# Performance work log

Hardware: AMD Instinct MI355X
Metric: run time of the kernel (lower is better)

Reference implementation:

```python
import jax, jax.numpy as jnp
import numpy as np

M_MODES = 12
N_PHOTONS = 6  # input_state = [1]*6 + [0]*6


def _glynn_signs(n):
    # All delta in {+1,-1}^n with delta_0 = +1 : 2^(n-1) sign vectors.
    k = np.arange(2 ** (n - 1))
    bits = (k[:, None] >> np.arange(n - 1)[None, :]) & 1  # [S, n-1]
    signs = np.concatenate([np.ones((k.size, 1)), 1.0 - 2.0 * bits], axis=1)
    parity = np.prod(signs, axis=1)  # [S]
    return jnp.asarray(signs, jnp.float32), jnp.asarray(parity, jnp.float32)


def _batched_permanent(Msub):
    # Glynn formula: perm(M) = 2^(1-n) * sum_delta prod(delta) * prod_j sum_i delta_i M_ij
    n = Msub.shape[-1]
    signs, parity = _glynn_signs(n)
    signs = signs.astype(Msub.dtype)
    # [..., S, n] row-sums under each sign vector
    rowsums = jnp.einsum('sn,...nj->...sj', signs, Msub)
    prods = jnp.prod(rowsums, axis=-1)  # [..., S]
    perm = jnp.einsum('s,...s->...', parity.astype(Msub.dtype), prods)
    return perm / (2.0 ** (n - 1))


def _feature_unitaries(x, A, B):
    # U(x) = A @ diag(exp(i x)) @ B  (phase-shifter layer between fixed interferometers)
    ph = jnp.exp(1j * x.astype(jnp.complex64))  # [N, m]
    return jnp.einsum('ab,nb,bc->nac', A, ph, B)  # [N, m, m]


def setup_inputs() -> dict:
    key = jax.random.key(0)
    k1, k2, k3, k4 = jax.random.split(key, 4)
    x1 = jax.random.normal(k1, (384, M_MODES), jnp.float32)
    x2 = jax.random.normal(k2, (384, M_MODES), jnp.float32)
    # Fixed Haar-random unitaries for the interferometer meshes
    rng = np.random.default_rng(0)
    A = np.linalg.qr(rng.normal(size=(M_MODES, M_MODES)) + 1j * rng.normal(size=(M_MODES, M_MODES)))[0]
    B = np.linalg.qr(rng.normal(size=(M_MODES, M_MODES)) + 1j * rng.normal(size=(M_MODES, M_MODES)))[0]
    return {
        'x1': x1, 'x2': x2,
        'A_re': jnp.asarray(A.real, jnp.float32), 'A_im': jnp.asarray(A.imag, jnp.float32),
        'B_re': jnp.asarray(B.real, jnp.float32), 'B_im': jnp.asarray(B.imag, jnp.float32),
    }


def reference(x1, x2, A_re, A_im, B_re, B_im):
    A = (A_re + 1j * A_im).astype(jnp.complex64)
    B = (B_re + 1j * B_im).astype(jnp.complex64)
    U1 = _feature_unitaries(x1, A, B)  # [N1, m, m]
    U2 = _feature_unitaries(x2, A, B)  # [N2, m, m]
    n = N_PHOTONS
    # W = U(x2)^dag U(x1); amplitude = perm(W[s_idx, s_idx]) with s_idx = first n modes
    # (input_state = [1]*n + [0]*(m-n), all factorials = 1)
    Wsub = jnp.einsum('jka,ikb->ijab', jnp.conj(U2[:, :, :n]), U1[:, :, :n])  # [N1,N2,n,n]
    amp = _batched_permanent(Wsub)  # [N1, N2] complex
    K = jnp.abs(amp) ** 2
    return K.astype(jnp.float32)
```

## Files before the change

### kernel.cpp

```cpp
#include <hip/hip_runtime.h>


#define NS 384
#define MM 12
#define NP 6
#define TS 16
#define SV_STRIDE 148

struct c32 { float x, y; };

__device__ __forceinline__ c32 cmul(c32 a, c32 b) {
    c32 r;
    r.x = fmaf(a.x, b.x, -a.y * b.y);
    r.y = fmaf(a.x, b.y,  a.y * b.x);
    return r;
}

__global__ void build_V_kernel(const float* __restrict__ x1,
                               const float* __restrict__ x2,
                               const float* __restrict__ Ar, const float* __restrict__ Ai,
                               const float* __restrict__ Br, const float* __restrict__ Bi,
                               float* __restrict__ V1, float* __restrict__ V2c) {
    int idx = blockIdx.x * blockDim.x + threadIdx.x;
    if (idx >= 2 * NS * NP * 2) return;
    int ah = idx & 1;
    int rest = idx >> 1;
    int c = rest % NP; rest /= NP;
    int s = rest % NS;
    int half = rest / NS;
    const float* x = half ? x2 : x1;

    float tr[MM], ti[MM];
#pragma unroll
    for (int b = 0; b < MM; ++b) {
        float sv, cv;
        __sincosf(x[s * MM + b], &sv, &cv);
        float br = Br[b * MM + c], bi = Bi[b * MM + c];
        tr[b] = fmaf(cv, br, -sv * bi);
        ti[b] = fmaf(cv, bi,  sv * br);
    }

    float* V = half ? V2c : V1;
    float sgn = half ? -1.f : 1.f;
#pragma unroll
    for (int a0 = 0; a0 < NP; ++a0) {
        int a = ah * NP + a0;
        float ure = 0.f, uim = 0.f;
#pragma unroll
        for (int b = 0; b < MM; ++b) {
            float ar = Ar[a * MM + b], ai = Ai[a * MM + b];
            ure = fmaf(ar, tr[b], fmaf(-ai, ti[b], ure));
            uim = fmaf(ar, ti[b], fmaf( ai, tr[b], uim));
        }
        int off = ((s * MM + a) * NP + c) * 2;
        V[off]     = ure;
        V[off + 1] = sgn * uim;
    }
}

__device__ __forceinline__ c32 tree_prod(const c32 rs[NP]) {
    c32 p01 = cmul(rs[0], rs[1]);
    c32 p23 = cmul(rs[2], rs[3]);
    c32 p45 = cmul(rs[4], rs[5]);
    return cmul(cmul(p01, p23), p45);
}

__global__ __launch_bounds__(256) void perm_kernel(const float* __restrict__ V1g,
                                                   const float* __restrict__ V2g,
                                                   float* __restrict__ out) {
    __shared__ __align__(16) float sV1[TS * SV_STRIDE];
    __shared__ __align__(16) float sV2[TS * SV_STRIDE];
    const int i0 = blockIdx.y * TS;
    const int j0 = blockIdx.x * TS;
    const int tid = threadIdx.x;

    for (int idx = tid; idx < 2 * TS * 36; idx += 256) {
        int which = idx >= TS * 36;
        int rem = which ? idx - TS * 36 : idx;
        int s = rem / 36, q = rem - s * 36;
        const float* src = which ? (V2g + (j0 + s) * 144) : (V1g + (i0 + s) * 144);
        float4 v = *(const float4*)(src + q * 4);
        float* dst = (which ? sV2 : sV1) + s * SV_STRIDE + q * 4;
        *(float4*)dst = v;
    }
    __syncthreads();

    const int tx = tid & 15, ty = tid >> 4;
    const float* v1 = sV1 + ty * SV_STRIDE;
    const float* v2 = sV2 + tx * SV_STRIDE;

    c32 W[NP][NP];
#pragma unroll
    for (int a = 0; a < NP; ++a)
#pragma unroll
        for (int b = 0; b < NP; ++b) { W[a][b].x = 0.f; W[a][b].y = 0.f; }

#pragma unroll
    for (int k = 0; k < MM; ++k) {
        float4 p1[3], p2[3];
#pragma unroll
        for (int q = 0; q < 3; ++q) {
            p1[q] = *(const float4*)(v1 + k * 12 + q * 4);
            p2[q] = *(const float4*)(v2 + k * 12 + q * 4);
        }
        const float* f1 = (const float*)p1;
        const float* f2 = (const float*)p2;
#pragma unroll
        for (int a = 0; a < NP; ++a) {
            float a2x = f2[2 * a], a2y = f2[2 * a + 1];
#pragma unroll
            for (int b = 0; b < NP; ++b) {
                float a1x = f1[2 * b], a1y = f1[2 * b + 1];
                W[a][b].x = fmaf(a2x, a1x, fmaf(-a2y, a1y, W[a][b].x));
                W[a][b].y = fmaf(a2x, a1y, fmaf( a2y, a1x, W[a][b].y));
            }
        }
    }

    c32 base[NP];
#pragma unroll
    for (int b = 0; b < NP; ++b) {
        base[b] = W[0][b];
#pragma unroll
        for (int a = 1; a < NP; ++a) { base[b].x += W[a][b].x; base[b].y += W[a][b].y; }
    }

    c32 rs[4][NP];
#pragma unroll
    for (int b = 0; b < NP; ++b) {
        rs[0][b] = base[b];
        rs[1][b].x = fmaf(-2.f, W[4][b].x, base[b].x);
        rs[1][b].y = fmaf(-2.f, W[4][b].y, base[b].y);
        rs[2][b].x = fmaf(-2.f, W[5][b].x, base[b].x);
        rs[2][b].y = fmaf(-2.f, W[5][b].y, base[b].y);
        rs[3][b].x = fmaf(-2.f, W[5][b].x, rs[1][b].x);
        rs[3][b].y = fmaf(-2.f, W[5][b].y, rs[1][b].y);
    }
    float accx[4], accy[4];
#pragma unroll
    for (int ch = 0; ch < 4; ++ch) {
        c32 p = tree_prod(rs[ch]);
        accx[ch] = p.x; accy[ch] = p.y;
    }

    unsigned st = 0;
#pragma unroll
    for (int u = 1; u < 8; ++u) {
        const int bitpos = __builtin_ctz(u);
        const int r = bitpos + 1;
        float cf = ((st >> bitpos) & 1) ? 2.f : -2.f;
        st ^= (1u << bitpos);
        float sgn_u = (u & 1) ? -1.f : 1.f;
#pragma unroll
        for (int ch = 0; ch < 4; ++ch) {
#pragma unroll
            for (int b = 0; b < NP; ++b) {
                rs[ch][b].x = fmaf(cf, W[r][b].x, rs[ch][b].x);
                rs[ch][b].y = fmaf(cf, W[r][b].y, rs[ch][b].y);
            }
            c32 p = tree_prod(rs[ch]);
            accx[ch] = fmaf(sgn_u, p.x, accx[ch]);
            accy[ch] = fmaf(sgn_u, p.y, accy[ch]);
        }
    }

    float ax = accx[0] - accx[1] - accx[2] + accx[3];
    float ay = accy[0] - accy[1] - accy[2] + accy[3];
    float K = fmaf(ax, ax, ay * ay) * (1.f / 1024.f);
    out[(i0 + ty) * NS + (j0 + tx)] = K;
}

extern "C" void kernel_launch(void* const* d_in, const int* in_sizes, int n_in,
                              void* d_out, int out_size, void* d_ws, size_t ws_size,
                              hipStream_t stream) {
    const float* x1 = (const float*)d_in[0];
    const float* x2 = (const float*)d_in[1];
    const float* Ar = (const float*)d_in[2];
    const float* Ai = (const float*)d_in[3];
    const float* Br = (const float*)d_in[4];
    const float* Bi = (const float*)d_in[5];
    float* out = (float*)d_out;

    float* V1  = (float*)d_ws;
    float* V2c = V1 + NS * MM * NP * 2;

    int total = 2 * NS * NP * 2;
    build_V_kernel<<<(total + 255) / 256, 256, 0, stream>>>(x1, x2, Ar, Ai, Br, Bi, V1, V2c);

    dim3 grid(NS / TS, NS / TS);
    perm_kernel<<<grid, 256, 0, stream>>>(V1, V2c, out);
}
```

Baseline: 80.73 us.

## Use packed float2 FMA vectors and widen build_V parallelism to one thread per element

Rewrites the complex arithmetic in both kernels with 2-wide float vector types and elementwise FMA, so the compiler can emit packed FP32 instructions (v_pk_fma_f32 on CDNA). This is meant to roughly halve the VALU instruction count in the permanent and Gram accumulation loops. The build_V kernel now uses one thread per output element instead of one per half-row, giving more parallelism at the cost of recomputing sincos and the B product per thread. The packed operations may need extra register moves for the swizzled operands, which could eat into the saving.

```diff
diff --git a/kernel.cpp b/kernel.cpp
--- a/kernel.cpp
+++ b/kernel.cpp
@@ -1,5 +1,7 @@
 #include <hip/hip_runtime.h>
 
+
+typedef float v2f __attribute__((ext_vector_type(2)));
 
 #define NS 384
 #define MM 12
@@ -7,13 +9,13 @@
 #define TS 16
 #define SV_STRIDE 148
 
-struct c32 { float x, y; };
-
-__device__ __forceinline__ c32 cmul(c32 a, c32 b) {
-    c32 r;
-    r.x = fmaf(a.x, b.x, -a.y * b.y);
-    r.y = fmaf(a.x, b.y,  a.y * b.x);
-    return r;
+__device__ __forceinline__ v2f cmul(v2f a, v2f b) {
+    v2f r = (v2f){a.x, a.x} * b;
+    return __builtin_elementwise_fma((v2f){a.y, a.y}, (v2f){-b.y, b.x}, r);
+}
+__device__ __forceinline__ v2f cmac(v2f acc, v2f a, v2f b) {
+    acc = __builtin_elementwise_fma((v2f){a.x, a.x}, b, acc);
+    return __builtin_elementwise_fma((v2f){a.y, a.y}, (v2f){-b.y, b.x}, acc);
 }
 
 __global__ void build_V_kernel(const float* __restrict__ x1,
@@ -22,46 +24,33 @@
                                const float* __restrict__ Br, const float* __restrict__ Bi,
                                float* __restrict__ V1, float* __restrict__ V2c) {
     int idx = blockIdx.x * blockDim.x + threadIdx.x;
-    if (idx >= 2 * NS * NP * 2) return;
-    int ah = idx & 1;
-    int rest = idx >> 1;
-    int c = rest % NP; rest /= NP;
-    int s = rest % NS;
-    int half = rest / NS;
+    if (idx >= 2 * NS * MM * NP) return;
+    int c = idx % NP;  int rest = idx / NP;
+    int a = rest % MM; rest /= MM;
+    int s = rest % NS; int half = rest / NS;
     const float* x = half ? x2 : x1;
 
-    float tr[MM], ti[MM];
+    v2f u = {0.f, 0.f};
 #pragma unroll
     for (int b = 0; b < MM; ++b) {
         float sv, cv;
         __sincosf(x[s * MM + b], &sv, &cv);
-        float br = Br[b * MM + c], bi = Bi[b * MM + c];
-        tr[b] = fmaf(cv, br, -sv * bi);
-        ti[b] = fmaf(cv, bi,  sv * br);
+        v2f ph = {cv, sv};
+        v2f Bv = {Br[b * MM + c], Bi[b * MM + c]};
+        v2f t  = cmul(ph, Bv);
+        v2f Av = {Ar[a * MM + b], Ai[a * MM + b]};
+        u = cmac(u, Av, t);
     }
-
     float* V = half ? V2c : V1;
-    float sgn = half ? -1.f : 1.f;
-#pragma unroll
-    for (int a0 = 0; a0 < NP; ++a0) {
-        int a = ah * NP + a0;
-        float ure = 0.f, uim = 0.f;
-#pragma unroll
-        for (int b = 0; b < MM; ++b) {
-            float ar = Ar[a * MM + b], ai = Ai[a * MM + b];
-            ure = fmaf(ar, tr[b], fmaf(-ai, ti[b], ure));
-            uim = fmaf(ar, ti[b], fmaf( ai, tr[b], uim));
-        }
-        int off = ((s * MM + a) * NP + c) * 2;
-        V[off]     = ure;
-        V[off + 1] = sgn * uim;
-    }
+    int off = ((s * MM + a) * NP + c) * 2;
+    V[off]     = u.x;
+    V[off + 1] = half ? -u.y : u.y;
 }
 
-__device__ __forceinline__ c32 tree_prod(const c32 rs[NP]) {
-    c32 p01 = cmul(rs[0], rs[1]);
-    c32 p23 = cmul(rs[2], rs[3]);
-    c32 p45 = cmul(rs[4], rs[5]);
+__device__ __forceinline__ v2f tree_prod(const v2f rs[NP]) {
+    v2f p01 = cmul(rs[0], rs[1]);
+    v2f p23 = cmul(rs[2], rs[3]);
+    v2f p45 = cmul(rs[4], rs[5]);
     return cmul(cmul(p01, p23), p45);
 }
 
@@ -89,59 +78,46 @@
     const float* v1 = sV1 + ty * SV_STRIDE;
     const float* v2 = sV2 + tx * SV_STRIDE;
 
-    c32 W[NP][NP];
+    v2f W[NP][NP];
 #pragma unroll
     for (int a = 0; a < NP; ++a)
 #pragma unroll
-        for (int b = 0; b < NP; ++b) { W[a][b].x = 0.f; W[a][b].y = 0.f; }
+        for (int b = 0; b < NP; ++b) W[a][b] = (v2f){0.f, 0.f};
 
 #pragma unroll
     for (int k = 0; k < MM; ++k) {
-        float4 p1[3], p2[3];
+        const v2f* c1 = (const v2f*)(v1 + k * 12);
+        const v2f* c2 = (const v2f*)(v2 + k * 12);
+        v2f a1[NP], a2[NP];
 #pragma unroll
-        for (int q = 0; q < 3; ++q) {
-            p1[q] = *(const float4*)(v1 + k * 12 + q * 4);
-            p2[q] = *(const float4*)(v2 + k * 12 + q * 4);
-        }
-        const float* f1 = (const float*)p1;
-        const float* f2 = (const float*)p2;
+        for (int b = 0; b < NP; ++b) { a1[b] = c1[b]; a2[b] = c2[b]; }
 #pragma unroll
-        for (int a = 0; a < NP; ++a) {
-            float a2x = f2[2 * a], a2y = f2[2 * a + 1];
+        for (int a = 0; a < NP; ++a)
 #pragma unroll
-            for (int b = 0; b < NP; ++b) {
-                float a1x = f1[2 * b], a1y = f1[2 * b + 1];
-                W[a][b].x = fmaf(a2x, a1x, fmaf(-a2y, a1y, W[a][b].x));
-                W[a][b].y = fmaf(a2x, a1y, fmaf( a2y, a1x, W[a][b].y));
-            }
-        }
+            for (int b = 0; b < NP; ++b)
+                W[a][b] = cmac(W[a][b], a2[a], a1[b]);
     }
 
-    c32 base[NP];
+    v2f base[NP];
 #pragma unroll
     for (int b = 0; b < NP; ++b) {
         base[b] = W[0][b];
 #pragma unroll
-        for (int a = 1; a < NP; ++a) { base[b].x += W[a][b].x; base[b].y += W[a][b].y; }
+        for (int a = 1; a < NP; ++a) base[b] += W[a][b];
     }
 
-    c32 rs[4][NP];
+    v2f rs[4][NP];
 #pragma unroll
     for (int b = 0; b < NP; ++b) {
+        v2f m2 = {-2.f, -2.f};
         rs[0][b] = base[b];
-        rs[1][b].x = fmaf(-2.f, W[4][b].x, base[b].x);
-        rs[1][b].y = fmaf(-2.f, W[4][b].y, base[b].y);
-        rs[2][b].x = fmaf(-2.f, W[5][b].x, base[b].x);
-        rs[2][b].y = fmaf(-2.f, W[5][b].y, base[b].y);
-        rs[3][b].x = fmaf(-2.f, W[5][b].x, rs[1][b].x);
-        rs[3][b].y = fmaf(-2.f, W[5][b].y, rs[1][b].y);
+        rs[1][b] = __builtin_elementwise_fma(m2, W[4][b], base[b]);
+        rs[2][b] = __builtin_elementwise_fma(m2, W[5][b], base[b]);
+        rs[3][b] = __builtin_elementwise_fma(m2, W[5][b], rs[1][b]);
     }
-    float accx[4], accy[4];
+    v2f acc[4];
 #pragma unroll
-    for (int ch = 0; ch < 4; ++ch) {
-        c32 p = tree_prod(rs[ch]);
-        accx[ch] = p.x; accy[ch] = p.y;
-    }
+    for (int ch = 0; ch < 4; ++ch) acc[ch] = tree_prod(rs[ch]);
 
     unsigned st = 0;
 #pragma unroll
@@ -151,22 +127,20 @@
         float cf = ((st >> bitpos) & 1) ? 2.f : -2.f;
         st ^= (1u << bitpos);
         float sgn_u = (u & 1) ? -1.f : 1.f;
+        v2f cfv = {cf, cf};
+        v2f sgv = {sgn_u, sgn_u};
 #pragma unroll
         for (int ch = 0; ch < 4; ++ch) {
 #pragma unroll
-            for (int b = 0; b < NP; ++b) {
-                rs[ch][b].x = fmaf(cf, W[r][b].x, rs[ch][b].x);
-                rs[ch][b].y = fmaf(cf, W[r][b].y, rs[ch][b].y);
-            }
-            c32 p = tree_prod(rs[ch]);
-            accx[ch] = fmaf(sgn_u, p.x, accx[ch]);
-            accy[ch] = fmaf(sgn_u, p.y, accy[ch]);
+            for (int b = 0; b < NP; ++b)
+                rs[ch][b] = __builtin_elementwise_fma(cfv, W[r][b], rs[ch][b]);
+            v2f p = tree_prod(rs[ch]);
+            acc[ch] = __builtin_elementwise_fma(sgv, p, acc[ch]);
         }
     }
 
-    float ax = accx[0] - accx[1] - accx[2] + accx[3];
-    float ay = accy[0] - accy[1] - accy[2] + accy[3];
-    float K = fmaf(ax, ax, ay * ay) * (1.f / 1024.f);
+    v2f aa = acc[0] - acc[1] - acc[2] + acc[3];
+    float K = fmaf(aa.x, aa.x, aa.y * aa.y) * (1.f / 1024.f);
     out[(i0 + ty) * NS + (j0 + tx)] = K;
 }
 
@@ -184,7 +158,7 @@
     float* V1  = (float*)d_ws;
     float* V2c = V1 + NS * MM * NP * 2;
 
-    int total = 2 * NS * NP * 2;
+    int total = 2 * NS * MM * NP;
     build_V_kernel<<<(total + 255) / 256, 256, 0, stream>>>(x1, x2, Ar, Ai, Br, Bi, V1, V2c);
 
     dim3 grid(NS / TS, NS / TS);
```

Result: faster. 78.49 us (-2.8%).
